# Kernel optimization log

Hardware: AMD Instinct MI355X
Metric: run time of the kernel (lower is better)

## Reference

```python
import jax, jax.numpy as jnp
import numpy as np

NUM_HEADS = 16
NUM_KV_HEADS = 4
HEAD_DIM = 128
SCALE = 0.08838834764831845  # 1/sqrt(128)
T = 4096
NUM_SLOTS = 8192
BLOCK_LENGTH = 32


def setup_inputs() -> dict:
    key = jax.random.key(0)
    k1, k2, k3 = jax.random.split(key, 3)
    return {
        "q": jax.random.normal(k1, (T, NUM_HEADS * HEAD_DIM), dtype=jnp.float32),
        "k": jax.random.normal(k2, (T, NUM_KV_HEADS * HEAD_DIM), dtype=jnp.float32),
        "v": jax.random.normal(k3, (T, NUM_KV_HEADS * HEAD_DIM), dtype=jnp.float32),
        "k_cache": jnp.zeros((NUM_SLOTS, NUM_KV_HEADS * HEAD_DIM), dtype=jnp.float32),
        "v_cache": jnp.zeros((NUM_SLOTS, NUM_KV_HEADS * HEAD_DIM), dtype=jnp.float32),
        "slot_mapping": jnp.arange(T, dtype=jnp.int32),
        "block_length": BLOCK_LENGTH,
    }


def reference(q, k, v, k_cache, v_cache, slot_mapping, block_length):
    # PREFILL path of BlockAttention: scatter KV into paged cache, then
    # staircase (block-causal) sparse attention over the prefill tokens.
    t = q.shape[0]
    qh = q.reshape(t, NUM_HEADS, HEAD_DIM)          # (T, H, D)
    kh = k.reshape(t, NUM_KV_HEADS, HEAD_DIM)       # (T, Hkv, D)
    vh = v.reshape(t, NUM_KV_HEADS, HEAD_DIM)

    # store_kvcache: scatter flattened K/V rows into cache slots
    kc = k_cache.at[slot_mapping].set(k)
    vc = v_cache.at[slot_mapping].set(v)

    # GQA: replicate KV heads across query-head groups
    g = NUM_HEADS // NUM_KV_HEADS
    kr = jnp.repeat(kh, g, axis=1)                  # (T, H, D)
    vr = jnp.repeat(vh, g, axis=1)

    # staircase mask: query in block i attends to all keys in blocks <= i
    blk = jnp.arange(t) // block_length
    allowed = blk[None, :] <= blk[:, None]          # (Tq, Tk)

    scores = jnp.einsum("qhd,khd->hqk", qh, kr) * SCALE   # (H, T, T)
    scores = jnp.where(allowed[None, :, :], scores, jnp.float32(-1e30))
    probs = jax.nn.softmax(scores, axis=-1)
    o = jnp.einsum("hqk,khd->qhd", probs, vr)       # (T, H, D)
    return o.reshape(t, NUM_HEADS * HEAD_DIM), kc, vc
```

## Files before the change

### kernel.cpp

```cpp
#include <hip/hip_runtime.h>
#include <stdint.h>
#include <type_traits>

#define NH 16
#define NKV 4
#define HD 128
#define QS (NH*HD)
#define KSR (NKV*HD)
#define SCALE 0.08838834764831845f
#define CT 32

typedef float f32x4 __attribute__((ext_vector_type(4)));
typedef __bf16 bf16x8 __attribute__((ext_vector_type(8)));
typedef __bf16 bf16x4 __attribute__((ext_vector_type(4)));

__device__ __forceinline__ void gll16(const void* g, void* l) {
  __builtin_amdgcn_global_load_lds((const __attribute__((address_space(1))) void*)g,
                                   (__attribute__((address_space(3))) void*)l, 16, 0, 0);
}

__global__ __launch_bounds__(256) void prepass_kernel(
    const float* __restrict__ k, const float* __restrict__ v,
    __bf16* __restrict__ kb, __bf16* __restrict__ vb) {
  const int tid = threadIdx.x;
  const int kvh = blockIdx.x >> 6;
  const int kt = blockIdx.x & 63;
  const size_t ibase = (size_t)(kvh * 64 + kt) << 13;
#pragma unroll
  for (int rep = 0; rep < 8; ++rep) {
    int i = tid + rep * 256;
    int row = i >> 5;
    int c4 = (i & 31) << 2;
    f32x4 a = *(const f32x4*)(k + (size_t)(kt * 64 + row) * KSR + kvh * HD + c4);
    bf16x4 t;
    t[0] = (__bf16)(a[0] * SCALE); t[1] = (__bf16)(a[1] * SCALE);
    t[2] = (__bf16)(a[2] * SCALE); t[3] = (__bf16)(a[3] * SCALE);
    *(bf16x4*)&kb[ibase + row * 128 + (c4 ^ ((row & 7) << 3))] = t;
    f32x4 b = *(const f32x4*)(v + (size_t)(kt * 64 + row) * KSR + kvh * HD + c4);
#pragma unroll
    for (int e = 0; e < 4; ++e) {
      int d = c4 + e;
      vb[ibase + d * 64 + (row ^ ((d & 7) << 3))] = (__bf16)b[e];
    }
  }
}

__global__ __launch_bounds__(256, 2) void attn_kernel(
    const float* __restrict__ q, const __bf16* __restrict__ kb,
    const __bf16* __restrict__ vb, float* __restrict__ o,
    __bf16* __restrict__ opart, float2* __restrict__ stats, int mode) {
  __shared__ __bf16 Kt[2][64][128];
  __shared__ __bf16 VT[2][128][64];
  __shared__ __bf16 Pt[4][32][64];

  const int tid = threadIdx.x;
  const int lane = tid & 63;
  const int wid = tid >> 6;
  const int g = lane >> 4, r = lane & 15;
  const int h = blockIdx.x & 15;
  const int u = blockIdx.x >> 4;

  int qt, c;
  if (mode) { qt = 31 - u; c = 0; }
  else if (u < 16) { qt = 31 - u; c = 0; }
  else { qt = 47 - u; c = (u < 32) ? 1 : 0; }

  const int kvh = h >> 2;
  const int nch = (!mode && qt >= 16) ? 2 : 1;
  const int t0 = c * CT;
  const int maxt = mode ? 64 : CT;
  int ntb = 2 * qt + 2 - t0;
  if (ntb > maxt) ntb = maxt;
  const int qrow0 = qt * 128 + wid * 32;
  const int limit32 = qt * 4 + wid + 1;

  bf16x8 qf[2][4];
#pragma unroll
  for (int qh = 0; qh < 2; ++qh)
#pragma unroll
    for (int ks = 0; ks < 4; ++ks) {
      const float* src = q + (size_t)(qrow0 + qh * 16 + r) * QS + h * HD + 32 * ks + 8 * g;
      f32x4 a = *(const f32x4*)src, b = *(const f32x4*)(src + 4);
      bf16x8 tt;
      tt[0] = (__bf16)a[0]; tt[1] = (__bf16)a[1]; tt[2] = (__bf16)a[2]; tt[3] = (__bf16)a[3];
      tt[4] = (__bf16)b[0]; tt[5] = (__bf16)b[1]; tt[6] = (__bf16)b[2]; tt[7] = (__bf16)b[3];
      qf[qh][ks] = tt;
    }

  f32x4 oacc[2][8];
#pragma unroll
  for (int qh = 0; qh < 2; ++qh)
#pragma unroll
    for (int nt = 0; nt < 8; ++nt) oacc[qh][nt] = (f32x4){0.f, 0.f, 0.f, 0.f};
  float mrun[2] = {-1e30f, -1e30f}, lrun[2] = {0.f, 0.f};

  auto stage = [&](int ktg, int buf) {
    const __bf16* gK = kb + (((size_t)(kvh * 64 + ktg)) << 13) + tid * 8;
    const __bf16* gV = vb + (((size_t)(kvh * 64 + ktg)) << 13) + tid * 8;
    __bf16* lK = &Kt[buf][0][0] + tid * 8;
    __bf16* lV = &VT[buf][0][0] + tid * 8;
#pragma unroll
    for (int i = 0; i < 4; ++i) {
      gll16(gK + i * 2048, lK + i * 2048);
      gll16(gV + i * 2048, lV + i * 2048);
    }
  };

  auto qk_phase = [&](auto NGC, int buf) {
    constexpr int NG = decltype(NGC)::value;
    f32x4 sacc[2][NG];
#pragma unroll
    for (int nt2 = 0; nt2 < NG; ++nt2) {
      bf16x8 kf[4];
#pragma unroll
      for (int ks = 0; ks < 4; ++ks)
        kf[ks] = *(const bf16x8*)&Kt[buf][16 * nt2 + r][(32 * ks + 8 * g) ^ ((r & 7) << 3)];
      __builtin_amdgcn_s_setprio(1);
#pragma unroll
      for (int qh = 0; qh < 2; ++qh) {
        f32x4 cacc = (f32x4){0.f, 0.f, 0.f, 0.f};
#pragma unroll
        for (int ks = 0; ks < 4; ++ks)
          cacc = __builtin_amdgcn_mfma_f32_16x16x32_bf16(kf[ks], qf[qh][ks], cacc, 0, 0, 0);
        sacc[qh][nt2] = cacc;
      }
      __builtin_amdgcn_s_setprio(0);
    }
#pragma unroll
    for (int qh = 0; qh < 2; ++qh) {
      float mx = -1e30f;
#pragma unroll
      for (int nt2 = 0; nt2 < NG; ++nt2)
#pragma unroll
        for (int j = 0; j < 4; ++j) mx = fmaxf(mx, sacc[qh][nt2][j]);
      mx = fmaxf(mx, __shfl_xor(mx, 16));
      mx = fmaxf(mx, __shfl_xor(mx, 32));
      float mold = mrun[qh];
      float mnew = fmaxf(mold, mx);
      unsigned long long chg = __ballot(mx > mold);
      mrun[qh] = mnew;
      float ts = 0.f;
#pragma unroll
      for (int nt2 = 0; nt2 < NG; ++nt2) {
        bf16x4 pw;
#pragma unroll
        for (int j = 0; j < 4; ++j) {
          float p = __expf(sacc[qh][nt2][j] - mnew);
          ts += p;
          pw[j] = (__bf16)p;
        }
        *(bf16x4*)&Pt[wid][qh * 16 + r][(16 * nt2 + 4 * g) ^ ((r & 7) << 3)] = pw;
      }
      ts += __shfl_xor(ts, 16);
      ts += __shfl_xor(ts, 32);
      if (chg) {
        float cf = __expf(mold - mnew);
        lrun[qh] = lrun[qh] * cf + ts;
#pragma unroll
        for (int j = 0; j < 4; ++j) {
          float cfj = __shfl(cf, 20 * g + j);
#pragma unroll
          for (int nt = 0; nt < 8; ++nt) oacc[qh][nt][j] *= cfj;
        }
      } else {
        lrun[qh] += ts;
      }
    }
  };

  auto pv_phase = [&](auto NGC, int buf) {
    constexpr int NG = decltype(NGC)::value;
    bf16x8 pa[2][NG / 2];
#pragma unroll
    for (int qh = 0; qh < 2; ++qh)
#pragma unroll
      for (int kc = 0; kc < NG / 2; ++kc)
        pa[qh][kc] = *(const bf16x8*)&Pt[wid][qh * 16 + r][(32 * kc + 8 * g) ^ ((r & 7) << 3)];
    __builtin_amdgcn_s_setprio(1);
#pragma unroll
    for (int nt = 0; nt < 8; ++nt) {
#pragma unroll
      for (int kc = 0; kc < NG / 2; ++kc) {
        bf16x8 vf = *(const bf16x8*)&VT[buf][16 * nt + r][(32 * kc + 8 * g) ^ ((r & 7) << 3)];
#pragma unroll
        for (int qh = 0; qh < 2; ++qh)
          oacc[qh][nt] = __builtin_amdgcn_mfma_f32_16x16x32_bf16(pa[qh][kc], vf, oacc[qh][nt], 0, 0, 0);
      }
    }
    __builtin_amdgcn_s_setprio(0);
  };

  stage(t0, 0);

  for (int j = 0; j < ntb; ++j) {
    const int buf = j & 1;
    if (j + 1 < ntb) {
      stage(t0 + j + 1, buf ^ 1);
      asm volatile("s_waitcnt vmcnt(8)" ::: "memory");
    } else {
      asm volatile("s_waitcnt vmcnt(0)" ::: "memory");
    }
    __builtin_amdgcn_s_barrier();
    __builtin_amdgcn_sched_barrier(0);
    const int rem = limit32 - 2 * (t0 + j);
    if (rem >= 2) {
      qk_phase(std::integral_constant<int, 4>{}, buf);
      pv_phase(std::integral_constant<int, 4>{}, buf);
    } else if (rem == 1) {
      qk_phase(std::integral_constant<int, 2>{}, buf);
      pv_phase(std::integral_constant<int, 2>{}, buf);
    }
    __builtin_amdgcn_sched_barrier(0);
    __builtin_amdgcn_s_barrier();
    __builtin_amdgcn_sched_barrier(0);
  }

  if (nch == 1) {
#pragma unroll
    for (int qh = 0; qh < 2; ++qh) {
      float invl = 1.0f / lrun[qh];
#pragma unroll
      for (int j = 0; j < 4; ++j) {
        float iv = __shfl(invl, 20 * g + j);
        int row = qrow0 + qh * 16 + 4 * g + j;
#pragma unroll
        for (int nt = 0; nt < 8; ++nt)
          o[(size_t)row * QS + h * HD + 16 * nt + r] = oacc[qh][nt][j] * iv;
      }
    }
  } else {
    const int slot = (h * 16 + (qt - 16)) * 2 + c;
    __bf16* op = opart + (size_t)slot * 16384;
#pragma unroll
    for (int qh = 0; qh < 2; ++qh) {
#pragma unroll
      for (int j = 0; j < 4; ++j) {
        int rl = wid * 32 + qh * 16 + 4 * g + j;
#pragma unroll
        for (int nt = 0; nt < 8; ++nt)
          op[rl * 128 + 16 * nt + r] = (__bf16)oacc[qh][nt][j];
      }
      if (g == 0)
        stats[slot * 128 + wid * 32 + qh * 16 + r] = make_float2(mrun[qh], lrun[qh]);
    }
  }
}

__global__ __launch_bounds__(256) void merge_kernel(
    const __bf16* __restrict__ opart, const float2* __restrict__ stats,
    float* __restrict__ o) {
  const int bi = blockIdx.x;
  const int qtr = bi >> 7;
  const int rm = bi & 127;
  const int h = rm >> 3;
  const int rb = rm & 7;
  const int t = threadIdx.x;
  const int rl = rb * 16 + (t >> 4);
  const int d8 = (t & 15) << 3;
  const int slot = (h * 16 + qtr) * 2;
  float2 s0 = stats[slot * 128 + rl];
  float2 s1 = stats[(slot + 1) * 128 + rl];
  float M = fmaxf(s0.x, s1.x);
  float w0 = __expf(s0.x - M), w1 = __expf(s1.x - M);
  float inv = 1.0f / (s0.y * w0 + s1.y * w1);
  bf16x8 a = *(const bf16x8*)&opart[(size_t)slot * 16384 + rl * 128 + d8];
  bf16x8 b = *(const bf16x8*)&opart[(size_t)(slot + 1) * 16384 + rl * 128 + d8];
  float* dst = o + (size_t)((16 + qtr) * 128 + rl) * QS + h * HD + d8;
  f32x4 o0, o1;
#pragma unroll
  for (int e = 0; e < 4; ++e) o0[e] = ((float)a[e] * w0 + (float)b[e] * w1) * inv;
#pragma unroll
  for (int e = 0; e < 4; ++e) o1[e] = ((float)a[4 + e] * w0 + (float)b[4 + e] * w1) * inv;
  *(f32x4*)dst = o0;
  *(f32x4*)(dst + 4) = o1;
}

__global__ void copy_caches_kernel(const f32x4* __restrict__ kc, const f32x4* __restrict__ vc,
                                   f32x4* __restrict__ okc, f32x4* __restrict__ ovc, int n4) {
  int i = blockIdx.x * blockDim.x + threadIdx.x;
  int stride = gridDim.x * blockDim.x;
  for (; i < n4; i += stride) {
    okc[i] = kc[i];
    ovc[i] = vc[i];
  }
}

__global__ void scatter_kernel(const float* __restrict__ k, const float* __restrict__ v,
                               const int* __restrict__ slot, float* __restrict__ okc,
                               float* __restrict__ ovc, int t) {
  int i = blockIdx.x * blockDim.x + threadIdx.x;
  int row = i >> 7, c = i & 127;
  if (row < t) {
    int s = slot[row];
    ((f32x4*)okc)[(size_t)s * 128 + c] = ((const f32x4*)k)[(size_t)row * 128 + c];
    ((f32x4*)ovc)[(size_t)s * 128 + c] = ((const f32x4*)v)[(size_t)row * 128 + c];
  }
}

extern "C" void kernel_launch(void* const* d_in, const int* in_sizes, int n_in,
                              void* d_out, int out_size, void* d_ws, size_t ws_size,
                              hipStream_t stream) {
  const float* q = (const float*)d_in[0];
  const float* k = (const float*)d_in[1];
  const float* v = (const float*)d_in[2];
  const float* kc = (const float*)d_in[3];
  const float* vc = (const float*)d_in[4];
  const int* slot = (const int*)d_in[5];

  const int t = in_sizes[0] / QS;
  const int nslots = in_sizes[3] / KSR;

  float* o = (float*)d_out;
  float* okc = o + (size_t)t * QS;
  float* ovc = okc + (size_t)nslots * KSR;

  __bf16* kb = (__bf16*)d_ws;
  __bf16* vb = kb + 2097152;
  const size_t off_op = (size_t)8 << 20;
  const size_t off_st = off_op + (size_t)512 * 16384 * 2;
  const size_t need_split = off_st + (size_t)512 * 128 * 8;
  __bf16* opart = (__bf16*)((char*)d_ws + off_op);
  float2* stats = (float2*)((char*)d_ws + off_st);

  const int mode = (ws_size >= need_split) ? 0 : 1;

  hipLaunchKernelGGL(prepass_kernel, dim3(256), dim3(256), 0, stream, k, v, kb, vb);
  hipLaunchKernelGGL(attn_kernel, dim3((mode ? 32 : 48) * 16), dim3(256), 0, stream,
                     q, kb, vb, o, opart, stats, mode);
  if (mode == 0)
    hipLaunchKernelGGL(merge_kernel, dim3(2048), dim3(256), 0, stream, opart, stats, o);

  int n4 = nslots * KSR / 4;
  hipLaunchKernelGGL(copy_caches_kernel, dim3(4096), dim3(256), 0, stream,
                     (const f32x4*)kc, (const f32x4*)vc, (f32x4*)okc, (f32x4*)ovc, n4);
  int nthreads = t * (KSR / 4);
  hipLaunchKernelGGL(scatter_kernel, dim3((nthreads + 255) / 256), dim3(256), 0, stream,
                     k, v, slot, okc, ovc, t);
}
```

Baseline: 259.6 us.

## Software-pipeline attention: overlap QK/softmax of next tile with PV of previous

Splits K and V staging so K is prefetched one tile ahead and V lags one tile. The loop now runs QK and softmax for tile j, then PV for tile j-1 with deferred rescaling, giving the MFMA units independent work while softmax runs. Folds log2(e) into the K prescale and switches exp to exp2 throughout, including the merge. Also rewrites the prepass so K and V writes are 16-byte vectorized. The cost is extra registers for the carried P fragments and a more complex prologue and epilogue.

```diff
diff --git a/kernel.cpp b/kernel.cpp
--- a/kernel.cpp
+++ b/kernel.cpp
@@ -8,6 +8,7 @@
 #define QS (NH*HD)
 #define KSR (NKV*HD)
 #define SCALE 0.08838834764831845f
+#define LOG2E 1.4426950408889634f
 #define CT 32
 
 typedef float f32x4 __attribute__((ext_vector_type(4)));
@@ -26,22 +27,27 @@
   const int kvh = blockIdx.x >> 6;
   const int kt = blockIdx.x & 63;
   const size_t ibase = (size_t)(kvh * 64 + kt) << 13;
-#pragma unroll
-  for (int rep = 0; rep < 8; ++rep) {
+  const float KS = SCALE * LOG2E;
+#pragma unroll
+  for (int rep = 0; rep < 4; ++rep) {
     int i = tid + rep * 256;
-    int row = i >> 5;
-    int c4 = (i & 31) << 2;
-    f32x4 a = *(const f32x4*)(k + (size_t)(kt * 64 + row) * KSR + kvh * HD + c4);
-    bf16x4 t;
-    t[0] = (__bf16)(a[0] * SCALE); t[1] = (__bf16)(a[1] * SCALE);
-    t[2] = (__bf16)(a[2] * SCALE); t[3] = (__bf16)(a[3] * SCALE);
-    *(bf16x4*)&kb[ibase + row * 128 + (c4 ^ ((row & 7) << 3))] = t;
-    f32x4 b = *(const f32x4*)(v + (size_t)(kt * 64 + row) * KSR + kvh * HD + c4);
-#pragma unroll
-    for (int e = 0; e < 4; ++e) {
-      int d = c4 + e;
-      vb[ibase + d * 64 + (row ^ ((d & 7) << 3))] = (__bf16)b[e];
-    }
+    int row = i >> 4, c8 = (i & 15) << 3;
+    const float* src = k + (size_t)(kt * 64 + row) * KSR + kvh * HD + c8;
+    f32x4 a = *(const f32x4*)src, b = *(const f32x4*)(src + 4);
+    bf16x8 t;
+#pragma unroll
+    for (int e = 0; e < 4; ++e) { t[e] = (__bf16)(a[e] * KS); t[4 + e] = (__bf16)(b[e] * KS); }
+    *(bf16x8*)&kb[ibase + row * 128 + (c8 ^ ((row & 7) << 3))] = t;
+  }
+#pragma unroll
+  for (int rep = 0; rep < 4; ++rep) {
+    int i = tid + rep * 256;
+    int d = i >> 3, k8 = (i & 7) << 3;
+    bf16x8 t;
+#pragma unroll
+    for (int w = 0; w < 8; ++w)
+      t[w] = (__bf16)v[(size_t)(kt * 64 + k8 + w) * KSR + kvh * HD + d];
+    *(bf16x8*)&vb[ibase + d * 64 + (k8 ^ ((d & 7) << 3))] = t;
   }
 }
 
@@ -82,8 +88,8 @@
       const float* src = q + (size_t)(qrow0 + qh * 16 + r) * QS + h * HD + 32 * ks + 8 * g;
       f32x4 a = *(const f32x4*)src, b = *(const f32x4*)(src + 4);
       bf16x8 tt;
-      tt[0] = (__bf16)a[0]; tt[1] = (__bf16)a[1]; tt[2] = (__bf16)a[2]; tt[3] = (__bf16)a[3];
-      tt[4] = (__bf16)b[0]; tt[5] = (__bf16)b[1]; tt[6] = (__bf16)b[2]; tt[7] = (__bf16)b[3];
+#pragma unroll
+      for (int e = 0; e < 4; ++e) { tt[e] = (__bf16)a[e]; tt[4 + e] = (__bf16)b[e]; }
       qf[qh][ks] = tt;
     }
 
@@ -94,21 +100,34 @@
     for (int nt = 0; nt < 8; ++nt) oacc[qh][nt] = (f32x4){0.f, 0.f, 0.f, 0.f};
   float mrun[2] = {-1e30f, -1e30f}, lrun[2] = {0.f, 0.f};
 
-  auto stage = [&](int ktg, int buf) {
+  f32x4 sacc[2][4];
+  bf16x8 pa[2][2];
+  float cfv[2];
+  bool dor[2] = {false, false};
+
+  auto stageK = [&](int ktg, int buf) {
     const __bf16* gK = kb + (((size_t)(kvh * 64 + ktg)) << 13) + tid * 8;
+    __bf16* lK = &Kt[buf][0][0] + tid * 8;
+#pragma unroll
+    for (int i = 0; i < 4; ++i) gll16(gK + i * 2048, lK + i * 2048);
+  };
+  auto stageV = [&](int ktg, int buf) {
     const __bf16* gV = vb + (((size_t)(kvh * 64 + ktg)) << 13) + tid * 8;
-    __bf16* lK = &Kt[buf][0][0] + tid * 8;
     __bf16* lV = &VT[buf][0][0] + tid * 8;
 #pragma unroll
-    for (int i = 0; i < 4; ++i) {
-      gll16(gK + i * 2048, lK + i * 2048);
-      gll16(gV + i * 2048, lV + i * 2048);
-    }
-  };
-
-  auto qk_phase = [&](auto NGC, int buf) {
+    for (int i = 0; i < 4; ++i) gll16(gV + i * 2048, lV + i * 2048);
+  };
+
+  auto pa_load = [&]() {
+#pragma unroll
+    for (int qh = 0; qh < 2; ++qh)
+#pragma unroll
+      for (int kc = 0; kc < 2; ++kc)
+        pa[qh][kc] = *(const bf16x8*)&Pt[wid][qh * 16 + r][(32 * kc + 8 * g) ^ ((r & 7) << 3)];
+  };
+
+  auto qk = [&](auto NGC, int buf) {
     constexpr int NG = decltype(NGC)::value;
-    f32x4 sacc[2][NG];
 #pragma unroll
     for (int nt2 = 0; nt2 < NG; ++nt2) {
       bf16x8 kf[4];
@@ -126,13 +145,18 @@
       }
       __builtin_amdgcn_s_setprio(0);
     }
+  };
+
+  auto softmax_f = [&](auto NGC) {
+    constexpr int NG = decltype(NGC)::value;
 #pragma unroll
     for (int qh = 0; qh < 2; ++qh) {
-      float mx = -1e30f;
+      float mx = sacc[qh][0][0];
 #pragma unroll
       for (int nt2 = 0; nt2 < NG; ++nt2)
 #pragma unroll
-        for (int j = 0; j < 4; ++j) mx = fmaxf(mx, sacc[qh][nt2][j]);
+        for (int j = 0; j < 4; ++j)
+          if (nt2 || j) mx = fmaxf(mx, sacc[qh][nt2][j]);
       mx = fmaxf(mx, __shfl_xor(mx, 16));
       mx = fmaxf(mx, __shfl_xor(mx, 32));
       float mold = mrun[qh];
@@ -141,79 +165,126 @@
       mrun[qh] = mnew;
       float ts = 0.f;
 #pragma unroll
-      for (int nt2 = 0; nt2 < NG; ++nt2) {
+      for (int nt2 = 0; nt2 < 4; ++nt2) {
         bf16x4 pw;
-#pragma unroll
-        for (int j = 0; j < 4; ++j) {
-          float p = __expf(sacc[qh][nt2][j] - mnew);
-          ts += p;
-          pw[j] = (__bf16)p;
+        if (nt2 < NG) {
+#pragma unroll
+          for (int j = 0; j < 4; ++j) {
+            float p = exp2f(sacc[qh][nt2][j] - mnew);
+            ts += p;
+            pw[j] = (__bf16)p;
+          }
+        } else {
+#pragma unroll
+          for (int j = 0; j < 4; ++j) pw[j] = (__bf16)0.f;
         }
         *(bf16x4*)&Pt[wid][qh * 16 + r][(16 * nt2 + 4 * g) ^ ((r & 7) << 3)] = pw;
       }
       ts += __shfl_xor(ts, 16);
       ts += __shfl_xor(ts, 32);
       if (chg) {
-        float cf = __expf(mold - mnew);
+        float cf = exp2f(mold - mnew);
         lrun[qh] = lrun[qh] * cf + ts;
+        cfv[qh] = cf;
+        dor[qh] = true;
+      } else {
+        lrun[qh] += ts;
+        dor[qh] = false;
+      }
+    }
+  };
+
+  auto zero_fill = [&]() {
+    bf16x4 pw;
+#pragma unroll
+    for (int j = 0; j < 4; ++j) pw[j] = (__bf16)0.f;
+#pragma unroll
+    for (int qh = 0; qh < 2; ++qh)
+#pragma unroll
+      for (int nt2 = 0; nt2 < 4; ++nt2)
+        *(bf16x4*)&Pt[wid][qh * 16 + r][(16 * nt2 + 4 * g) ^ ((r & 7) << 3)] = pw;
+    dor[0] = dor[1] = false;
+  };
+
+  auto pv_f = [&](int vbuf) {
+    __builtin_amdgcn_s_setprio(1);
+#pragma unroll
+    for (int nt = 0; nt < 8; ++nt)
+#pragma unroll
+      for (int kc = 0; kc < 2; ++kc) {
+        bf16x8 vf = *(const bf16x8*)&VT[vbuf][16 * nt + r][(32 * kc + 8 * g) ^ ((r & 7) << 3)];
+#pragma unroll
+        for (int qh = 0; qh < 2; ++qh)
+          oacc[qh][nt] = __builtin_amdgcn_mfma_f32_16x16x32_bf16(pa[qh][kc], vf, oacc[qh][nt], 0, 0, 0);
+      }
+    __builtin_amdgcn_s_setprio(0);
+  };
+
+  auto rescale_f = [&]() {
+#pragma unroll
+    for (int qh = 0; qh < 2; ++qh)
+      if (dor[qh]) {
 #pragma unroll
         for (int j = 0; j < 4; ++j) {
-          float cfj = __shfl(cf, 20 * g + j);
+          float cfj = __shfl(cfv[qh], 20 * g + j);
 #pragma unroll
           for (int nt = 0; nt < 8; ++nt) oacc[qh][nt][j] *= cfj;
         }
-      } else {
-        lrun[qh] += ts;
-      }
-    }
-  };
-
-  auto pv_phase = [&](auto NGC, int buf) {
-    constexpr int NG = decltype(NGC)::value;
-    bf16x8 pa[2][NG / 2];
-#pragma unroll
-    for (int qh = 0; qh < 2; ++qh)
-#pragma unroll
-      for (int kc = 0; kc < NG / 2; ++kc)
-        pa[qh][kc] = *(const bf16x8*)&Pt[wid][qh * 16 + r][(32 * kc + 8 * g) ^ ((r & 7) << 3)];
-    __builtin_amdgcn_s_setprio(1);
-#pragma unroll
-    for (int nt = 0; nt < 8; ++nt) {
-#pragma unroll
-      for (int kc = 0; kc < NG / 2; ++kc) {
-        bf16x8 vf = *(const bf16x8*)&VT[buf][16 * nt + r][(32 * kc + 8 * g) ^ ((r & 7) << 3)];
-#pragma unroll
-        for (int qh = 0; qh < 2; ++qh)
-          oacc[qh][nt] = __builtin_amdgcn_mfma_f32_16x16x32_bf16(pa[qh][kc], vf, oacc[qh][nt], 0, 0, 0);
-      }
-    }
-    __builtin_amdgcn_s_setprio(0);
-  };
-
-  stage(t0, 0);
-
-  for (int j = 0; j < ntb; ++j) {
+      }
+  };
+
+  constexpr auto IC4 = std::integral_constant<int, 4>{};
+  constexpr auto IC2 = std::integral_constant<int, 2>{};
+
+  stageK(t0, 0);
+
+  {
+    if (1 < ntb) stageK(t0 + 1, 1);
+    stageV(t0, 0);
+    if (1 < ntb) asm volatile("s_waitcnt vmcnt(8)" ::: "memory");
+    else         asm volatile("s_waitcnt vmcnt(4)" ::: "memory");
+    __builtin_amdgcn_s_barrier();
+    const int rem = limit32 - 2 * t0;
+    if (rem >= 2)      { qk(IC4, 0); softmax_f(IC4); }
+    else if (rem == 1) { qk(IC2, 0); softmax_f(IC2); }
+    else               zero_fill();
+    __builtin_amdgcn_s_barrier();
+  }
+
+  for (int j = 1; j < ntb; ++j) {
     const int buf = j & 1;
     if (j + 1 < ntb) {
-      stage(t0 + j + 1, buf ^ 1);
+      stageK(t0 + j + 1, buf ^ 1);
+      stageV(t0 + j, buf);
       asm volatile("s_waitcnt vmcnt(8)" ::: "memory");
     } else {
-      asm volatile("s_waitcnt vmcnt(0)" ::: "memory");
+      stageV(t0 + j, buf);
+      asm volatile("s_waitcnt vmcnt(4)" ::: "memory");
     }
     __builtin_amdgcn_s_barrier();
-    __builtin_amdgcn_sched_barrier(0);
+    pa_load();
     const int rem = limit32 - 2 * (t0 + j);
     if (rem >= 2) {
-      qk_phase(std::integral_constant<int, 4>{}, buf);
-      pv_phase(std::integral_constant<int, 4>{}, buf);
+      qk(IC4, buf);
+      softmax_f(IC4);
+      pv_f(buf ^ 1);
+      rescale_f();
     } else if (rem == 1) {
-      qk_phase(std::integral_constant<int, 2>{}, buf);
-      pv_phase(std::integral_constant<int, 2>{}, buf);
-    }
-    __builtin_amdgcn_sched_barrier(0);
+      qk(IC2, buf);
+      softmax_f(IC2);
+      pv_f(buf ^ 1);
+      rescale_f();
+    } else {
+      zero_fill();
+      pv_f(buf ^ 1);
+    }
     __builtin_amdgcn_s_barrier();
-    __builtin_amdgcn_sched_barrier(0);
-  }
+  }
+
+  asm volatile("s_waitcnt vmcnt(0)" ::: "memory");
+  __builtin_amdgcn_s_barrier();
+  pa_load();
+  pv_f((ntb - 1) & 1);
 
   if (nch == 1) {
 #pragma unroll
@@ -261,7 +332,7 @@
   float2 s0 = stats[slot * 128 + rl];
   float2 s1 = stats[(slot + 1) * 128 + rl];
   float M = fmaxf(s0.x, s1.x);
-  float w0 = __expf(s0.x - M), w1 = __expf(s1.x - M);
+  float w0 = exp2f(s0.x - M), w1 = exp2f(s1.x - M);
   float inv = 1.0f / (s0.y * w0 + s1.y * w1);
   bf16x8 a = *(const bf16x8*)&opart[(size_t)slot * 16384 + rl * 128 + d8];
   bf16x8 b = *(const bf16x8*)&opart[(size_t)(slot + 1) * 16384 + rl * 128 + d8];
```

New measurement: 270.5 us. 1.04x slower.

## Switch attention to 32x32x16 MFMA with register-resident P via permlane swap

Applied to the files above, without the earlier changes.

The attention kernel moves from 16x16x32 to 32x32x16 bf16 MFMA tiles, so each wave handles 32 query rows with a single softmax state. The P matrix is now packed with v_cvt_pk_bf16 and rearranged in registers with v_permlane32_swap, which removes the LDS round trip through the Pt buffer. Softmax uses exp2 with log2(e) folded into the K prescale, and the prepass writes vectorized 8-wide bf16 stores for both K and transposed V. Together these cut LDS traffic, shuffles and per-element conversion, at the cost of higher register pressure per wave and reliance on gfx950-specific instructions.

```diff
diff --git a/kernel.cpp b/kernel.cpp
--- a/kernel.cpp
+++ b/kernel.cpp
@@ -8,15 +8,24 @@
 #define QS (NH*HD)
 #define KSR (NKV*HD)
 #define SCALE 0.08838834764831845f
+#define LOG2E 1.4426950408889634f
 #define CT 32
 
 typedef float f32x4 __attribute__((ext_vector_type(4)));
+typedef float f32x16 __attribute__((ext_vector_type(16)));
 typedef __bf16 bf16x8 __attribute__((ext_vector_type(8)));
 typedef __bf16 bf16x4 __attribute__((ext_vector_type(4)));
+typedef unsigned int u32x4 __attribute__((ext_vector_type(4)));
 
 __device__ __forceinline__ void gll16(const void* g, void* l) {
   __builtin_amdgcn_global_load_lds((const __attribute__((address_space(1))) void*)g,
                                    (__attribute__((address_space(3))) void*)l, 16, 0, 0);
+}
+
+__device__ __forceinline__ unsigned cvt_pk_bf16(float a, float b) {
+  unsigned r;
+  asm("v_cvt_pk_bf16_f32 %0, %1, %2" : "=v"(r) : "v"(a), "v"(b));
+  return r;
 }
 
 __global__ __launch_bounds__(256) void prepass_kernel(
@@ -26,22 +35,27 @@
   const int kvh = blockIdx.x >> 6;
   const int kt = blockIdx.x & 63;
   const size_t ibase = (size_t)(kvh * 64 + kt) << 13;
-#pragma unroll
-  for (int rep = 0; rep < 8; ++rep) {
+  const float KS = SCALE * LOG2E;
+#pragma unroll
+  for (int rep = 0; rep < 4; ++rep) {
     int i = tid + rep * 256;
-    int row = i >> 5;
-    int c4 = (i & 31) << 2;
-    f32x4 a = *(const f32x4*)(k + (size_t)(kt * 64 + row) * KSR + kvh * HD + c4);
-    bf16x4 t;
-    t[0] = (__bf16)(a[0] * SCALE); t[1] = (__bf16)(a[1] * SCALE);
-    t[2] = (__bf16)(a[2] * SCALE); t[3] = (__bf16)(a[3] * SCALE);
-    *(bf16x4*)&kb[ibase + row * 128 + (c4 ^ ((row & 7) << 3))] = t;
-    f32x4 b = *(const f32x4*)(v + (size_t)(kt * 64 + row) * KSR + kvh * HD + c4);
-#pragma unroll
-    for (int e = 0; e < 4; ++e) {
-      int d = c4 + e;
-      vb[ibase + d * 64 + (row ^ ((d & 7) << 3))] = (__bf16)b[e];
-    }
+    int row = i >> 4, c8 = (i & 15) << 3;
+    const float* src = k + (size_t)(kt * 64 + row) * KSR + kvh * HD + c8;
+    f32x4 a = *(const f32x4*)src, b = *(const f32x4*)(src + 4);
+    bf16x8 t;
+#pragma unroll
+    for (int e = 0; e < 4; ++e) { t[e] = (__bf16)(a[e] * KS); t[4 + e] = (__bf16)(b[e] * KS); }
+    *(bf16x8*)&kb[ibase + row * 128 + (c8 ^ ((row & 7) << 3))] = t;
+  }
+#pragma unroll
+  for (int rep = 0; rep < 4; ++rep) {
+    int i = tid + rep * 256;
+    int d = i >> 3, k8 = (i & 7) << 3;
+    bf16x8 t;
+#pragma unroll
+    for (int w = 0; w < 8; ++w)
+      t[w] = (__bf16)v[(size_t)(kt * 64 + k8 + w) * KSR + kvh * HD + d];
+    *(bf16x8*)&vb[ibase + d * 64 + (k8 ^ ((d & 7) << 3))] = t;
   }
 }
 
@@ -51,12 +65,11 @@
     __bf16* __restrict__ opart, float2* __restrict__ stats, int mode) {
   __shared__ __bf16 Kt[2][64][128];
   __shared__ __bf16 VT[2][128][64];
-  __shared__ __bf16 Pt[4][32][64];
 
   const int tid = threadIdx.x;
   const int lane = tid & 63;
   const int wid = tid >> 6;
-  const int g = lane >> 4, r = lane & 15;
+  const int nq = lane & 31, hi = lane >> 5;
   const int h = blockIdx.x & 15;
   const int u = blockIdx.x >> 4;
 
@@ -73,176 +86,157 @@
   if (ntb > maxt) ntb = maxt;
   const int qrow0 = qt * 128 + wid * 32;
   const int limit32 = qt * 4 + wid + 1;
-
-  bf16x8 qf[2][4];
-#pragma unroll
-  for (int qh = 0; qh < 2; ++qh)
-#pragma unroll
-    for (int ks = 0; ks < 4; ++ks) {
-      const float* src = q + (size_t)(qrow0 + qh * 16 + r) * QS + h * HD + 32 * ks + 8 * g;
-      f32x4 a = *(const f32x4*)src, b = *(const f32x4*)(src + 4);
-      bf16x8 tt;
-      tt[0] = (__bf16)a[0]; tt[1] = (__bf16)a[1]; tt[2] = (__bf16)a[2]; tt[3] = (__bf16)a[3];
-      tt[4] = (__bf16)b[0]; tt[5] = (__bf16)b[1]; tt[6] = (__bf16)b[2]; tt[7] = (__bf16)b[3];
-      qf[qh][ks] = tt;
+  const int swz = (nq & 7) << 3;
+
+  bf16x8 qf[8];
+  {
+    const float* qp = q + (size_t)(qrow0 + nq) * QS + h * HD + hi * 8;
+#pragma unroll
+    for (int ks = 0; ks < 8; ++ks) {
+      f32x4 a = *(const f32x4*)(qp + ks * 16);
+      f32x4 b = *(const f32x4*)(qp + ks * 16 + 4);
+      bf16x8 t;
+#pragma unroll
+      for (int e = 0; e < 4; ++e) { t[e] = (__bf16)a[e]; t[4 + e] = (__bf16)b[e]; }
+      qf[ks] = t;
     }
-
-  f32x4 oacc[2][8];
-#pragma unroll
-  for (int qh = 0; qh < 2; ++qh)
-#pragma unroll
-    for (int nt = 0; nt < 8; ++nt) oacc[qh][nt] = (f32x4){0.f, 0.f, 0.f, 0.f};
-  float mrun[2] = {-1e30f, -1e30f}, lrun[2] = {0.f, 0.f};
-
-  auto stage = [&](int ktg, int buf) {
-    const __bf16* gK = kb + (((size_t)(kvh * 64 + ktg)) << 13) + tid * 8;
-    const __bf16* gV = vb + (((size_t)(kvh * 64 + ktg)) << 13) + tid * 8;
+  }
+
+  f32x16 oacc[4];
+#pragma unroll
+  for (int vt = 0; vt < 4; ++vt)
+#pragma unroll
+    for (int e = 0; e < 16; ++e) oacc[vt][e] = 0.f;
+  float mrun = -1e30f, lrun = 0.f;
+
+  auto stageKV = [&](int ktg, int buf) {
+    const size_t gb = ((size_t)(kvh * 64 + ktg)) << 13;
+    const __bf16* gK = kb + gb + tid * 8;
+    const __bf16* gV = vb + gb + tid * 8;
     __bf16* lK = &Kt[buf][0][0] + tid * 8;
     __bf16* lV = &VT[buf][0][0] + tid * 8;
 #pragma unroll
-    for (int i = 0; i < 4; ++i) {
-      gll16(gK + i * 2048, lK + i * 2048);
-      gll16(gV + i * 2048, lV + i * 2048);
+    for (int i = 0; i < 4; ++i) gll16(gK + i * 2048, lK + i * 2048);
+#pragma unroll
+    for (int i = 0; i < 4; ++i) gll16(gV + i * 2048, lV + i * 2048);
+  };
+
+  auto tile = [&](auto NGC, int buf) {
+    constexpr int NG = decltype(NGC)::value;
+    f32x16 sacc[NG];
+#pragma unroll
+    for (int grp = 0; grp < NG; ++grp) {
+      f32x16 cc;
+#pragma unroll
+      for (int e = 0; e < 16; ++e) cc[e] = 0.f;
+      __builtin_amdgcn_s_setprio(1);
+#pragma unroll
+      for (int ks = 0; ks < 8; ++ks) {
+        bf16x8 kf = *(const bf16x8*)&Kt[buf][grp * 32 + nq][(ks * 16 + hi * 8) ^ swz];
+        cc = __builtin_amdgcn_mfma_f32_32x32x16_bf16(kf, qf[ks], cc, 0, 0, 0);
+      }
+      __builtin_amdgcn_s_setprio(0);
+      sacc[grp] = cc;
     }
-  };
-
-  auto qk_phase = [&](auto NGC, int buf) {
-    constexpr int NG = decltype(NGC)::value;
-    f32x4 sacc[2][NG];
-#pragma unroll
-    for (int nt2 = 0; nt2 < NG; ++nt2) {
-      bf16x8 kf[4];
-#pragma unroll
-      for (int ks = 0; ks < 4; ++ks)
-        kf[ks] = *(const bf16x8*)&Kt[buf][16 * nt2 + r][(32 * ks + 8 * g) ^ ((r & 7) << 3)];
-      __builtin_amdgcn_s_setprio(1);
-#pragma unroll
-      for (int qh = 0; qh < 2; ++qh) {
-        f32x4 cacc = (f32x4){0.f, 0.f, 0.f, 0.f};
-#pragma unroll
-        for (int ks = 0; ks < 4; ++ks)
-          cacc = __builtin_amdgcn_mfma_f32_16x16x32_bf16(kf[ks], qf[qh][ks], cacc, 0, 0, 0);
-        sacc[qh][nt2] = cacc;
-      }
-      __builtin_amdgcn_s_setprio(0);
+    float mx = sacc[0][0];
+#pragma unroll
+    for (int grp = 0; grp < NG; ++grp)
+#pragma unroll
+      for (int e = 0; e < 16; ++e)
+        if (grp || e) mx = fmaxf(mx, sacc[grp][e]);
+    mx = fmaxf(mx, __shfl_xor(mx, 32));
+    float mold = mrun;
+    float mnew = fmaxf(mold, mx);
+    unsigned long long chg = __ballot(mx > mold);
+    mrun = mnew;
+    float ts = 0.f;
+    unsigned pk[NG * 8];
+#pragma unroll
+    for (int grp = 0; grp < NG; ++grp)
+#pragma unroll
+      for (int w = 0; w < 8; ++w) {
+        float p0 = exp2f(sacc[grp][2 * w] - mnew);
+        float p1 = exp2f(sacc[grp][2 * w + 1] - mnew);
+        ts += p0 + p1;
+        pk[grp * 8 + w] = cvt_pk_bf16(p0, p1);
+      }
+    ts += __shfl_xor(ts, 32);
+    if (chg) {
+      float cf = exp2f(mold - mnew);
+      lrun = lrun * cf + ts;
+#pragma unroll
+      for (int vt = 0; vt < 4; ++vt)
+#pragma unroll
+        for (int e = 0; e < 16; ++e) oacc[vt][e] *= cf;
+    } else {
+      lrun += ts;
     }
-#pragma unroll
-    for (int qh = 0; qh < 2; ++qh) {
-      float mx = -1e30f;
-#pragma unroll
-      for (int nt2 = 0; nt2 < NG; ++nt2)
-#pragma unroll
-        for (int j = 0; j < 4; ++j) mx = fmaxf(mx, sacc[qh][nt2][j]);
-      mx = fmaxf(mx, __shfl_xor(mx, 16));
-      mx = fmaxf(mx, __shfl_xor(mx, 32));
-      float mold = mrun[qh];
-      float mnew = fmaxf(mold, mx);
-      unsigned long long chg = __ballot(mx > mold);
-      mrun[qh] = mnew;
-      float ts = 0.f;
-#pragma unroll
-      for (int nt2 = 0; nt2 < NG; ++nt2) {
-        bf16x4 pw;
-#pragma unroll
-        for (int j = 0; j < 4; ++j) {
-          float p = __expf(sacc[qh][nt2][j] - mnew);
-          ts += p;
-          pw[j] = (__bf16)p;
-        }
-        *(bf16x4*)&Pt[wid][qh * 16 + r][(16 * nt2 + 4 * g) ^ ((r & 7) << 3)] = pw;
-      }
-      ts += __shfl_xor(ts, 16);
-      ts += __shfl_xor(ts, 32);
-      if (chg) {
-        float cf = __expf(mold - mnew);
-        lrun[qh] = lrun[qh] * cf + ts;
-#pragma unroll
-        for (int j = 0; j < 4; ++j) {
-          float cfj = __shfl(cf, 20 * g + j);
-#pragma unroll
-          for (int nt = 0; nt < 8; ++nt) oacc[qh][nt][j] *= cfj;
-        }
-      } else {
-        lrun[qh] += ts;
-      }
-    }
-  };
-
-  auto pv_phase = [&](auto NGC, int buf) {
-    constexpr int NG = decltype(NGC)::value;
-    bf16x8 pa[2][NG / 2];
-#pragma unroll
-    for (int qh = 0; qh < 2; ++qh)
-#pragma unroll
-      for (int kc = 0; kc < NG / 2; ++kc)
-        pa[qh][kc] = *(const bf16x8*)&Pt[wid][qh * 16 + r][(32 * kc + 8 * g) ^ ((r & 7) << 3)];
+    bf16x8 paf[NG * 2];
+#pragma unroll
+    for (int grp = 0; grp < NG; ++grp)
+#pragma unroll
+      for (int s = 0; s < 2; ++s) {
+        unsigned a0 = pk[grp * 8 + 4 * s + 0], a1 = pk[grp * 8 + 4 * s + 2];
+        unsigned b0 = pk[grp * 8 + 4 * s + 1], b1 = pk[grp * 8 + 4 * s + 3];
+        asm("v_permlane32_swap_b32 %0, %1" : "+v"(a0), "+v"(a1));
+        asm("v_permlane32_swap_b32 %0, %1" : "+v"(b0), "+v"(b1));
+        u32x4 uu;
+        uu[0] = a0; uu[1] = b0; uu[2] = a1; uu[3] = b1;
+        paf[grp * 2 + s] = __builtin_bit_cast(bf16x8, uu);
+      }
     __builtin_amdgcn_s_setprio(1);
 #pragma unroll
-    for (int nt = 0; nt < 8; ++nt) {
-#pragma unroll
-      for (int kc = 0; kc < NG / 2; ++kc) {
-        bf16x8 vf = *(const bf16x8*)&VT[buf][16 * nt + r][(32 * kc + 8 * g) ^ ((r & 7) << 3)];
-#pragma unroll
-        for (int qh = 0; qh < 2; ++qh)
-          oacc[qh][nt] = __builtin_amdgcn_mfma_f32_16x16x32_bf16(pa[qh][kc], vf, oacc[qh][nt], 0, 0, 0);
-      }
-    }
+    for (int vt = 0; vt < 4; ++vt)
+#pragma unroll
+      for (int s = 0; s < NG * 2; ++s) {
+        bf16x8 vf = *(const bf16x8*)&VT[buf][vt * 32 + nq][(s * 16 + hi * 8) ^ swz];
+        oacc[vt] = __builtin_amdgcn_mfma_f32_32x32x16_bf16(vf, paf[s], oacc[vt], 0, 0, 0);
+      }
     __builtin_amdgcn_s_setprio(0);
   };
 
-  stage(t0, 0);
-
+  stageKV(t0, 0);
   for (int j = 0; j < ntb; ++j) {
     const int buf = j & 1;
     if (j + 1 < ntb) {
-      stage(t0 + j + 1, buf ^ 1);
+      stageKV(t0 + j + 1, buf ^ 1);
       asm volatile("s_waitcnt vmcnt(8)" ::: "memory");
     } else {
       asm volatile("s_waitcnt vmcnt(0)" ::: "memory");
     }
     __builtin_amdgcn_s_barrier();
-    __builtin_amdgcn_sched_barrier(0);
     const int rem = limit32 - 2 * (t0 + j);
-    if (rem >= 2) {
-      qk_phase(std::integral_constant<int, 4>{}, buf);
-      pv_phase(std::integral_constant<int, 4>{}, buf);
-    } else if (rem == 1) {
-      qk_phase(std::integral_constant<int, 2>{}, buf);
-      pv_phase(std::integral_constant<int, 2>{}, buf);
-    }
-    __builtin_amdgcn_sched_barrier(0);
+    if (rem >= 2)      tile(std::integral_constant<int, 2>{}, buf);
+    else if (rem == 1) tile(std::integral_constant<int, 1>{}, buf);
     __builtin_amdgcn_s_barrier();
-    __builtin_amdgcn_sched_barrier(0);
   }
 
   if (nch == 1) {
-#pragma unroll
-    for (int qh = 0; qh < 2; ++qh) {
-      float invl = 1.0f / lrun[qh];
-#pragma unroll
-      for (int j = 0; j < 4; ++j) {
-        float iv = __shfl(invl, 20 * g + j);
-        int row = qrow0 + qh * 16 + 4 * g + j;
-#pragma unroll
-        for (int nt = 0; nt < 8; ++nt)
-          o[(size_t)row * QS + h * HD + 16 * nt + r] = oacc[qh][nt][j] * iv;
-      }
-    }
+    float inv = 1.0f / lrun;
+    float* op = o + (size_t)(qrow0 + nq) * QS + h * HD + 4 * hi;
+#pragma unroll
+    for (int vt = 0; vt < 4; ++vt)
+#pragma unroll
+      for (int G = 0; G < 4; ++G) {
+        f32x4 t;
+#pragma unroll
+        for (int e = 0; e < 4; ++e) t[e] = oacc[vt][4 * G + e] * inv;
+        *(f32x4*)(op + vt * 32 + 8 * G) = t;
+      }
   } else {
     const int slot = (h * 16 + (qt - 16)) * 2 + c;
-    __bf16* op = opart + (size_t)slot * 16384;
-#pragma unroll
-    for (int qh = 0; qh < 2; ++qh) {
-#pragma unroll
-      for (int j = 0; j < 4; ++j) {
-        int rl = wid * 32 + qh * 16 + 4 * g + j;
-#pragma unroll
-        for (int nt = 0; nt < 8; ++nt)
-          op[rl * 128 + 16 * nt + r] = (__bf16)oacc[qh][nt][j];
-      }
-      if (g == 0)
-        stats[slot * 128 + wid * 32 + qh * 16 + r] = make_float2(mrun[qh], lrun[qh]);
-    }
+    const int rl = wid * 32 + nq;
+    __bf16* op = opart + (size_t)slot * 16384 + rl * 128 + 4 * hi;
+#pragma unroll
+    for (int vt = 0; vt < 4; ++vt)
+#pragma unroll
+      for (int G = 0; G < 4; ++G) {
+        bf16x4 t;
+#pragma unroll
+        for (int e = 0; e < 4; ++e) t[e] = (__bf16)oacc[vt][4 * G + e];
+        *(bf16x4*)(op + vt * 32 + 8 * G) = t;
+      }
+    if (hi == 0) stats[slot * 128 + rl] = make_float2(mrun, lrun);
   }
 }
 
@@ -261,7 +255,7 @@
   float2 s0 = stats[slot * 128 + rl];
   float2 s1 = stats[(slot + 1) * 128 + rl];
   float M = fmaxf(s0.x, s1.x);
-  float w0 = __expf(s0.x - M), w1 = __expf(s1.x - M);
+  float w0 = exp2f(s0.x - M), w1 = exp2f(s1.x - M);
   float inv = 1.0f / (s0.y * w0 + s1.y * w1);
   bf16x8 a = *(const bf16x8*)&opart[(size_t)slot * 16384 + rl * 128 + d8];
   bf16x8 b = *(const bf16x8*)&opart[(size_t)(slot + 1) * 16384 + rl * 128 + d8];
```

New measurement: 249.5 us. -3.9%, faster.
